# Kernel tuning notes

Hardware: AMD Instinct MI355X
Metric: run time of the kernel (lower is better)

Reference implementation:

```python
import jax, jax.numpy as jnp
import numpy as np
from jax import lax

T, B, A_DIM, Z_DIM, K_MIX, HID = 128, 256, 16, 32, 8, 128
Q_REG = 1e-3
R_REG = 1e-3


def setup_inputs() -> dict:
    key = jax.random.key(0)
    ks = jax.random.split(key, 16)
    s = 1.0 / np.sqrt(HID)
    reg = 0.9
    as_ = jax.random.normal(ks[0], (T, B, A_DIM), dtype=jnp.float32)
    mat_A_K = (1.0 - reg) * jax.random.normal(ks[1], (K_MIX, Z_DIM, Z_DIM)) + reg * jnp.eye(Z_DIM)
    mat_C_K = (1.0 - reg) * jax.random.normal(ks[2], (K_MIX, A_DIM, Z_DIM)) + reg * jnp.eye(A_DIM, Z_DIM)
    # Cholesky factors of near-identity SPD matrices (as in torch init)
    Q_L = jnp.tril(0.05 * jax.random.normal(ks[3], (Z_DIM, Z_DIM))) + jnp.eye(Z_DIM)
    R_L = jnp.tril(0.05 * jax.random.normal(ks[4], (A_DIM, A_DIM))) + jnp.eye(A_DIM)
    init_mean = jnp.zeros((Z_DIM,), dtype=jnp.float32)
    init_cov = jnp.eye(Z_DIM, dtype=jnp.float32)
    u = lambda k, shp: jax.random.uniform(k, shp, minval=-s, maxval=s, dtype=jnp.float32)
    return dict(
        as_=as_, mat_A_K=mat_A_K, mat_C_K=mat_C_K, Q_L=Q_L, R_L=R_L,
        init_mean=init_mean, init_cov=init_cov,
        W_ih0=u(ks[5], (4 * HID, A_DIM)), W_hh0=u(ks[6], (4 * HID, HID)),
        b_ih0=u(ks[7], (4 * HID,)), b_hh0=u(ks[8], (4 * HID,)),
        W_ih1=u(ks[9], (4 * HID, HID)), W_hh1=u(ks[10], (4 * HID, HID)),
        b_ih1=u(ks[11], (4 * HID,)), b_hh1=u(ks[12], (4 * HID,)),
        W_out=u(ks[13], (K_MIX, HID)), b_out=u(ks[14], (K_MIX,)),
    )


def _lstm_cell(x, h, c, W_ih, W_hh, b_ih, b_hh):
    g = x @ W_ih.T + b_ih + h @ W_hh.T + b_hh
    i, f, gg, o = jnp.split(g, 4, axis=-1)
    c2 = jax.nn.sigmoid(f) * c + jax.nn.sigmoid(i) * jnp.tanh(gg)
    h2 = jax.nn.sigmoid(o) * jnp.tanh(c2)
    return h2, c2


def reference(as_, mat_A_K, mat_C_K, Q_L, R_L, init_mean, init_cov,
              W_ih0, W_hh0, b_ih0, b_hh0, W_ih1, W_hh1, b_ih1, b_hh1,
              W_out, b_out):
    Tn, Bn, a_dim = as_.shape
    Kn, z_dim, _ = mat_A_K.shape
    Hn = W_hh0.shape[1]
    Q = Q_L @ Q_L.T + Q_REG * jnp.eye(z_dim, dtype=as_.dtype)
    R = R_L @ R_L.T + R_REG * jnp.eye(a_dim, dtype=as_.dtype)

    def weight_model(a, h0, c0, h1, c1):
        h0, c0 = _lstm_cell(a, h0, c0, W_ih0, W_hh0, b_ih0, b_hh0)
        h1, c1 = _lstm_cell(h0, h1, c1, W_ih1, W_hh1, b_ih1, b_hh1)
        w = jax.nn.softmax(h1 @ W_out.T + b_out, axis=-1)
        return w, h0, c0, h1, c1

    def step(carry, a_t):
        mean_p, cov_p, weight, h0, c0, h1, c1 = carry
        # mixture matrices for this step (weight == previous step's w_next; ones at t=0)
        mat_A = jnp.einsum('bk,kij->bij', weight, mat_A_K)
        mat_C = jnp.einsum('bk,kij->bij', weight, mat_C_K)
        # sample_control = ('mean','mean'), observation_mask=None -> a = as_[t]
        w_next, h0, c0, h1, c1 = weight_model(a_t, h0, c0, h1, c1)
        mat_A_next = jnp.einsum('bk,kij->bij', w_next, mat_A_K)
        CP = mat_C @ cov_p                                   # (B,a,z)
        S = CP @ jnp.swapaxes(mat_C, 1, 2) + R               # (B,a,a)
        K_t = cov_p @ jnp.swapaxes(mat_C, 1, 2) @ jnp.linalg.inv(S)
        mean_t = mean_p + K_t @ (a_t[..., None] - mat_C @ mean_p)
        mean_p2 = mat_A_next @ mean_t
        cov_t = cov_p - K_t @ CP
        cov_t = 0.5 * (cov_t + jnp.swapaxes(cov_t, 1, 2))
        cov_p2 = mat_A_next @ cov_t @ jnp.swapaxes(mat_A_next, 1, 2) + Q
        cov_p2 = 0.5 * (cov_p2 + jnp.swapaxes(cov_p2, 1, 2))
        new_carry = (mean_p2, cov_p2, w_next, h0, c0, h1, c1)
        outs = (mean_t, cov_t, mean_p2, cov_p2, mat_A, mat_C, a_t)
        return new_carry, outs

    init = (
        jnp.broadcast_to(init_mean[None, :, None], (Bn, z_dim, 1)),
        jnp.broadcast_to(init_cov[None], (Bn, z_dim, z_dim)),
        jnp.ones((Bn, Kn), dtype=as_.dtype),
        jnp.zeros((Bn, Hn), dtype=as_.dtype), jnp.zeros((Bn, Hn), dtype=as_.dtype),
        jnp.zeros((Bn, Hn), dtype=as_.dtype), jnp.zeros((Bn, Hn), dtype=as_.dtype),
    )
    carry, ys = lax.scan(step, init, as_)
    means, covs, next_means, next_covs, mat_As, mat_Cs, a_seq = ys
    w_fin = carry[2]
    mat_A_fin = jnp.einsum('bk,kij->bij', w_fin, mat_A_K)
    mat_C_fin = jnp.einsum('bk,kij->bij', w_fin, mat_C_K)
    mat_As = jnp.concatenate([mat_As, mat_A_fin[None]], axis=0)   # (T+1,B,z,z)
    mat_Cs = jnp.concatenate([mat_Cs, mat_C_fin[None]], axis=0)   # (T+1,B,a,z)
    a_out = a_seq[:, None]                                        # (T,1,B,a) as in torch stack
    return means, covs, next_means, next_covs, mat_As, mat_Cs, a_out
```

## Files before the change

kernel.cpp:

```cpp
#include <hip/hip_runtime.h>
#include <hip/hip_fp16.h>
#include <math.h>

#define T_STEPS 128
#define B_SZ 256
#define AD 16
#define ZD 32
#define KM 8
#define HID 128
#define G4H 512
#define NTHR 512

#define WS_WQ   0
#define WS_WI0  98304
#define WS_BS0  102400
#define WS_BS1  102912
#define WS_Q    103424
#define WS_R    104448

typedef float f32x4 __attribute__((ext_vector_type(4)));

__device__ __forceinline__ unsigned pk16(float lo, float hi) {
  unsigned a = __half_as_ushort(__float2half_rn(lo));
  unsigned b = __half_as_ushort(__float2half_rn(hi));
  return a | (b << 16);
}

__global__ void ssm_prep_kernel(const float* __restrict__ Wih0, const float* __restrict__ Whh0,
                                const float* __restrict__ Wih1, const float* __restrict__ Whh1,
                                const float* __restrict__ bih0, const float* __restrict__ bhh0,
                                const float* __restrict__ bih1, const float* __restrict__ bhh1,
                                const float* __restrict__ QL, const float* __restrict__ RL,
                                float* __restrict__ ws) {
  unsigned* wsu = (unsigned*)ws;
  int tid = blockIdx.x * blockDim.x + threadIdx.x;
  int nt = gridDim.x * blockDim.x;
  for (int j = tid; j < G4H; j += nt) {
    for (int d4 = 0; d4 < 48; ++d4) {
      for (int m = 0; m < 4; ++m) {
        int dd = (d4 & 15) * 4 + m;
        const float* src = (d4 < 16) ? Whh0 : (d4 < 32) ? Wih1 : Whh1;
        wsu[WS_WQ + (d4 * 512 + j) * 4 + m] =
            pk16(src[j * 128 + 2 * dd], src[j * 128 + 2 * dd + 1]);
      }
    }
    for (int k = 0; k < 8; ++k)
      wsu[WS_WI0 + k * 512 + j] = pk16(Wih0[j * 16 + 2 * k], Wih0[j * 16 + 2 * k + 1]);
    ws[WS_BS0 + j] = bih0[j] + bhh0[j];
    ws[WS_BS1 + j] = bih1[j] + bhh1[j];
  }
  for (int e = tid; e < ZD * ZD; e += nt) {
    int i = e >> 5, j = e & 31;
    float s = 0.f;
    for (int k = 0; k < ZD; ++k) s += QL[i * ZD + k] * QL[j * ZD + k];
    if (i == j) s += 0.001f;
    ws[WS_Q + e] = s;
  }
  for (int e = tid; e < AD * AD; e += nt) {
    int i = e >> 4, j = e & 15;
    float s = 0.f;
    for (int k = 0; k < AD; ++k) s += RL[i * AD + k] * RL[j * AD + k];
    if (i == j) s += 0.001f;
    ws[WS_R + e] = s;
  }
}

__device__ __forceinline__ float sigm(float x) { return 1.0f / (1.0f + expf(-x)); }
__device__ __forceinline__ float dotv(f32x4 a, f32x4 b) {
  return a[0] * b[0] + a[1] * b[1] + a[2] * b[2] + a[3] * b[3];
}
__device__ __forceinline__ void st_nt(float* p, float v) { __builtin_nontemporal_store(v, p); }
__device__ __forceinline__ void st_nt4(float* p, f32x4 v) {
  __builtin_nontemporal_store(v, (f32x4*)p);
}

__device__ __forceinline__ float dot2f(unsigned a, unsigned b, float c) {
#if __has_builtin(__builtin_amdgcn_fdot2)
  typedef _Float16 h2 __attribute__((ext_vector_type(2)));
  union U { unsigned u; h2 h; };
  U ua, ub; ua.u = a; ub.u = b;
  return __builtin_amdgcn_fdot2(ua.h, ub.h, c, false);
#else
  union U { unsigned u; _Float16 h[2]; };
  U ua, ub; ua.u = a; ub.u = b;
  return c + (float)ua.h[0] * (float)ub.h[0] + (float)ua.h[1] * (float)ub.h[1];
#endif
}

struct alignas(16) LS {
  unsigned ap[8];
  unsigned h0p[64];
  unsigned h1p[64];
  float g[G4H];
  float lgp[16];
};

__global__ void __launch_bounds__(NTHR, 2) ssm_lstm_kernel(
    const float* __restrict__ as_, const float* __restrict__ AK, const float* __restrict__ CK,
    const float* __restrict__ Wout, const float* __restrict__ bout,
    const float* __restrict__ ws, float* __restrict__ out) {
  __shared__ LS s;
  const int tid = threadIdx.x;
  const int b = blockIdx.x;
  const unsigned* wsu = (const unsigned*)ws;
  const uint4* Wg = (const uint4*)(wsu + WS_WQ);
  const f32x4* AK4 = (const f32x4*)AK;
  const f32x4* CK4 = (const f32x4*)CK;

  float* o_As = out + (size_t)T_STEPS * B_SZ * ZD + (size_t)T_STEPS * B_SZ * ZD * ZD +
                (size_t)T_STEPS * B_SZ * ZD + (size_t)T_STEPS * B_SZ * ZD * ZD;
  float* o_Cs = o_As + (size_t)(T_STEPS + 1) * B_SZ * ZD * ZD;
  float* o_a = o_Cs + (size_t)(T_STEPS + 1) * B_SZ * AD * ZD;

  const uint4* h0p4 = (const uint4*)s.h0p;
  const uint4* h1p4 = (const uint4*)s.h1p;
  const uint4* ap4 = (const uint4*)s.ap;

  unsigned wi0r[8];
  #pragma unroll
  for (int k = 0; k < 8; ++k) wi0r[k] = wsu[WS_WI0 + k * 512 + tid];
  const float bs0r = ws[WS_BS0 + tid];
  const float bs1r = ws[WS_BS1 + tid];
  float woutr[8];
  #pragma unroll
  for (int gi = 0; gi < KM; ++gi) woutr[gi] = (tid < HID) ? Wout[gi * HID + tid] : 0.f;
  float boutr[8];
  #pragma unroll
  for (int k = 0; k < KM; ++k) boutr[k] = bout[k];

  float c0r = 0.f, c1r = 0.f;

  if (tid < 64) { s.h0p[tid] = 0u; s.h1p[tid] = 0u; }
  if (tid < AD) {
    float v = as_[(size_t)b * AD + tid];
    ((__half*)s.ap)[tid] = __float2half_rn(v);
    st_nt(&o_a[(size_t)b * AD + tid], v);
  }
  if (tid < 256) {
    f32x4 acc = {0.f, 0.f, 0.f, 0.f};
    #pragma unroll
    for (int k = 0; k < KM; ++k) acc += AK4[k * 256 + tid];
    st_nt4(&o_As[(size_t)b * 1024 + tid * 4], acc);
  } else if (tid < 384) {
    int idx = tid - 256;
    f32x4 acc = {0.f, 0.f, 0.f, 0.f};
    #pragma unroll
    for (int k = 0; k < KM; ++k) acc += CK4[k * 128 + idx];
    st_nt4(&o_Cs[(size_t)b * 512 + idx * 4], acc);
  }
  __syncthreads();

  for (int t = 0; t < T_STEPS; ++t) {
    const size_t tb2 = (size_t)(t + 1) * B_SZ + b;

    {
      float acc = bs0r;
      #pragma unroll
      for (int k4 = 0; k4 < 2; ++k4) {
        uint4 av = ap4[k4];
        acc = dot2f(av.x, wi0r[k4 * 4 + 0], acc);
        acc = dot2f(av.y, wi0r[k4 * 4 + 1], acc);
        acc = dot2f(av.z, wi0r[k4 * 4 + 2], acc);
        acc = dot2f(av.w, wi0r[k4 * 4 + 3], acc);
      }
      #pragma unroll
      for (int d4 = 0; d4 < 16; ++d4) {
        uint4 w = Wg[d4 * 512 + tid];
        uint4 hv = h0p4[d4];
        acc = dot2f(hv.x, w.x, acc);
        acc = dot2f(hv.y, w.y, acc);
        acc = dot2f(hv.z, w.z, acc);
        acc = dot2f(hv.w, w.w, acc);
      }
      s.g[tid] = acc;
    }
    __syncthreads();

    if (tid < HID) {
      float ig = sigm(s.g[tid]);
      float fg = sigm(s.g[HID + tid]);
      float gg = tanhf(s.g[2 * HID + tid]);
      float og = sigm(s.g[3 * HID + tid]);
      c0r = fg * c0r + ig * gg;
      ((__half*)s.h0p)[tid] = __float2half_rn(og * tanhf(c0r));
    }
    __syncthreads();

    {
      float acc = bs1r;
      #pragma unroll
      for (int d4 = 0; d4 < 16; ++d4) {
        uint4 w = Wg[(16 + d4) * 512 + tid];
        uint4 hv = h0p4[d4];
        acc = dot2f(hv.x, w.x, acc);
        acc = dot2f(hv.y, w.y, acc);
        acc = dot2f(hv.z, w.z, acc);
        acc = dot2f(hv.w, w.w, acc);
      }
      #pragma unroll
      for (int d4 = 0; d4 < 16; ++d4) {
        uint4 w = Wg[(32 + d4) * 512 + tid];
        uint4 hv = h1p4[d4];
        acc = dot2f(hv.x, w.x, acc);
        acc = dot2f(hv.y, w.y, acc);
        acc = dot2f(hv.z, w.z, acc);
        acc = dot2f(hv.w, w.w, acc);
      }
      s.g[tid] = acc;
    }
    __syncthreads();

    if (tid < HID) {
      float ig = sigm(s.g[tid]);
      float fg = sigm(s.g[HID + tid]);
      float gg = tanhf(s.g[2 * HID + tid]);
      float og = sigm(s.g[3 * HID + tid]);
      c1r = fg * c1r + ig * gg;
      float h1u = og * tanhf(c1r);
      ((__half*)s.h1p)[tid] = __float2half_rn(h1u);
      int w2 = tid >> 6, lane = tid & 63;
      #pragma unroll
      for (int gi = 0; gi < KM; ++gi) {
        float p = woutr[gi] * h1u;
        #pragma unroll
        for (int m = 32; m >= 1; m >>= 1) p += __shfl_xor(p, m);
        if (lane == 0) s.lgp[w2 * KM + gi] = p;
      }
    }
    __syncthreads();

    {
      float lg[KM];
      float mx = -1e30f;
      #pragma unroll
      for (int k = 0; k < KM; ++k) {
        lg[k] = s.lgp[k] + s.lgp[KM + k] + boutr[k];
        mx = fmaxf(mx, lg[k]);
      }
      float sum = 0.f;
      #pragma unroll
      for (int k = 0; k < KM; ++k) { lg[k] = expf(lg[k] - mx); sum += lg[k]; }
      float inv = 1.0f / sum;
      #pragma unroll
      for (int k = 0; k < KM; ++k) lg[k] *= inv;
      if (tid < 256) {
        f32x4 acc = {0.f, 0.f, 0.f, 0.f};
        #pragma unroll
        for (int k = 0; k < KM; ++k) acc += lg[k] * AK4[k * 256 + tid];
        st_nt4(&o_As[tb2 * 1024 + tid * 4], acc);
      } else if (tid < 384) {
        int idx = tid - 256;
        f32x4 acc = {0.f, 0.f, 0.f, 0.f};
        #pragma unroll
        for (int k = 0; k < KM; ++k) acc += lg[k] * CK4[k * 128 + idx];
        st_nt4(&o_Cs[tb2 * 512 + idx * 4], acc);
      } else if (tid >= 448 && tid < 448 + AD && t < T_STEPS - 1) {
        int i = tid - 448;
        float v = as_[tb2 * AD + i];
        ((__half*)s.ap)[i] = __float2half_rn(v);
        st_nt(&o_a[tb2 * AD + i], v);
      }
    }
    __syncthreads();
  }
}

struct alignas(16) KS {
  float P[ZD * 36];
  float An[ZD * 36];
  float Mt[ZD * 36];
  float MtT[ZD * 36];
  float Sy[ZD * 36];
  float ACt[ZD * 36];
  float Qs[ZD * 36];
  float C[AD * 36];
  float Aug[AD * 52];
  float Kk[ZD * 20];
  float Rs[AD * AD];
  float meanp[ZD], meant[ZD], r[AD], af[AD];
};

__global__ void __launch_bounds__(256, 1) ssm_kalman_kernel(
    const float* __restrict__ as_, const float* __restrict__ initm,
    const float* __restrict__ initc, const float* __restrict__ ws,
    float* __restrict__ out) {
  __shared__ KS s;
  const int l = threadIdx.x;
  const int b = blockIdx.x;
  const int i32 = l & 31, cq = l >> 5;
  const int i16 = l & 15, j16 = l >> 4;

  float* o_means = out;
  float* o_covs = o_means + (size_t)T_STEPS * B_SZ * ZD;
  float* o_nmean = o_covs + (size_t)T_STEPS * B_SZ * ZD * ZD;
  float* o_ncovs = o_nmean + (size_t)T_STEPS * B_SZ * ZD;
  const float* o_As = o_ncovs + (size_t)T_STEPS * B_SZ * ZD * ZD;
  const float* o_Cs = o_As + (size_t)(T_STEPS + 1) * B_SZ * ZD * ZD;

  f32x4* P4 = (f32x4*)s.P;
  f32x4* An4 = (f32x4*)s.An;
  f32x4* Mt4 = (f32x4*)s.Mt;
  f32x4* MtT4 = (f32x4*)s.MtT;
  f32x4* Sy4 = (f32x4*)s.Sy;
  f32x4* ACt4 = (f32x4*)s.ACt;
  f32x4* Q4 = (f32x4*)s.Qs;
  f32x4* C4 = (f32x4*)s.C;
  f32x4* Aug4 = (f32x4*)s.Aug;
  f32x4* Kk4 = (f32x4*)s.Kk;
  f32x4* af4 = (f32x4*)s.af;
  const f32x4* r4 = (const f32x4*)s.r;
  const f32x4* meanp4 = (const f32x4*)s.meanp;
  const f32x4* meant4 = (const f32x4*)s.meant;

  #pragma unroll
  for (int q = 0; q < 4; ++q) {
    int e = q * 256 + l;
    s.P[(e >> 5) * 36 + (e & 31)] = initc[e];
    s.Qs[(e >> 5) * 36 + (e & 31)] = ws[WS_Q + e];
  }
  s.Rs[l] = ws[WS_R + l];
  if (l < ZD) s.meanp[l] = initm[l];
  {
    const f32x4* gc = (const f32x4*)&o_Cs[(size_t)b * 512];
    if (l < 128) C4[(l >> 3) * 9 + (l & 7)] = gc[l];
    const f32x4* ga = (const f32x4*)&o_As[((size_t)B_SZ + b) * 1024];
    An4[(l >> 3) * 9 + (l & 7)] = ga[l];
    if (l < 4) af4[l] = ((const f32x4*)&as_[(size_t)b * AD])[l];
  }
  __syncthreads();

  for (int t = 0; t < T_STEPS; ++t) {
    const size_t tb = (size_t)t * B_SZ + b;
    const bool pf = (t < T_STEPS - 1);

    f32x4 pfC = {0, 0, 0, 0};
    f32x4 pfA = {0, 0, 0, 0};
    f32x4 pfa = {0, 0, 0, 0};
    if (pf) {
      if (l >= 128) pfC = ((const f32x4*)&o_Cs[(tb + B_SZ) * 512])[l - 128];
      pfA = ((const f32x4*)&o_As[(tb + 2 * B_SZ) * 1024])[l];
      if (l < 4) pfa = ((const f32x4*)&as_[(tb + B_SZ) * AD])[l];
    }

    {
      float a0 = 0.f, a1 = 0.f;
      #pragma unroll
      for (int k4 = 0; k4 < 8; ++k4) {
        f32x4 cr = C4[i16 * 9 + k4];
        a0 += dotv(cr, P4[j16 * 9 + k4]);
        a1 += dotv(cr, P4[(j16 + 16) * 9 + k4]);
      }
      s.Aug[i16 * 52 + AD + j16] = a0;
      s.Aug[i16 * 52 + AD + j16 + 16] = a1;
    }
    __syncthreads();

    {
      float acc = s.Rs[i16 * AD + j16];
      #pragma unroll
      for (int k4 = 0; k4 < 8; ++k4)
        acc += dotv(Aug4[i16 * 13 + 4 + k4], C4[j16 * 9 + k4]);
      s.Aug[i16 * 52 + j16] = acc;
      if (l >= 240) {
        int ii = l - 240;
        float rr = s.af[ii];
        #pragma unroll
        for (int k4 = 0; k4 < 8; ++k4) rr -= dotv(C4[ii * 9 + k4], meanp4[k4]);
        s.r[ii] = rr;
      }
    }
    __syncthreads();

    if (l < 64) {
      const int lc = (l < 48) ? l : 47;
      float col[16];
      #pragma unroll
      for (int i = 0; i < AD; ++i) col[i] = s.Aug[i * 52 + lc];
      #pragma unroll
      for (int j = 0; j < AD; ++j) {
        float pd = __shfl(col[j], j);
        float pinv = 1.0f / pd;
        float oldj = col[j];
        #pragma unroll
        for (int i = 0; i < AD; ++i) {
          if (i == j) continue;
          float fi = __shfl(col[i], j);
          col[i] = fmaf(-(fi * pinv), oldj, col[i]);
        }
        col[j] = oldj * pinv;
      }
      if (l >= AD && l < AD + ZD) {
        int rr = l - AD;
        f32x4 v0 = {col[0], col[1], col[2], col[3]};
        f32x4 v1 = {col[4], col[5], col[6], col[7]};
        f32x4 v2 = {col[8], col[9], col[10], col[11]};
        f32x4 v3 = {col[12], col[13], col[14], col[15]};
        Kk4[rr * 5 + 0] = v0;
        Kk4[rr * 5 + 1] = v1;
        Kk4[rr * 5 + 2] = v2;
        Kk4[rr * 5 + 3] = v3;
      }
    } else if (pf && l >= 128) {
      int idx = l - 128;
      C4[(idx >> 3) * 9 + (idx & 7)] = pfC;
    }
    __syncthreads();

    {
      f32x4 acc = {0.f, 0.f, 0.f, 0.f};
      #pragma unroll
      for (int k4 = 0; k4 < 4; ++k4) {
        f32x4 kv = Kk4[i32 * 5 + k4];
        #pragma unroll
        for (int kk = 0; kk < 4; ++kk) {
          f32x4 cpk = Aug4[(4 * k4 + kk) * 13 + 4 + cq];
          acc += kv[kk] * cpk;
        }
      }
      f32x4 mv = P4[i32 * 9 + cq] - acc;
      Mt4[i32 * 9 + cq] = mv;
      #pragma unroll
      for (int jj = 0; jj < 4; ++jj) s.MtT[(4 * cq + jj) * 36 + i32] = mv[jj];
    }
    __syncthreads();

    {
      f32x4 sv = 0.5f * (Mt4[i32 * 9 + cq] + MtT4[i32 * 9 + cq]);
      Sy4[i32 * 9 + cq] = sv;
      st_nt4(&o_covs[tb * 1024 + i32 * 32 + cq * 4], sv);
      if (l < ZD) {
        float acc = s.meanp[l];
        #pragma unroll
        for (int m = 0; m < 4; ++m) acc += dotv(Kk4[l * 5 + m], r4[m]);
        s.meant[l] = acc;
        st_nt(&o_means[tb * ZD + l], acc);
      }
    }
    __syncthreads();

    {
      float c0 = 0.f, c1 = 0.f, c2 = 0.f, c3 = 0.f;
      #pragma unroll
      for (int k4 = 0; k4 < 8; ++k4) {
        f32x4 an = An4[i32 * 9 + k4];
        c0 += dotv(an, Sy4[(4 * cq + 0) * 9 + k4]);
        c1 += dotv(an, Sy4[(4 * cq + 1) * 9 + k4]);
        c2 += dotv(an, Sy4[(4 * cq + 2) * 9 + k4]);
        c3 += dotv(an, Sy4[(4 * cq + 3) * 9 + k4]);
      }
      f32x4 v = {c0, c1, c2, c3};
      ACt4[i32 * 9 + cq] = v;
    }
    __syncthreads();

    {
      if (l < ZD) {
        float acc = 0.f;
        #pragma unroll
        for (int k4 = 0; k4 < 8; ++k4) acc += dotv(An4[l * 9 + k4], meant4[k4]);
        s.meanp[l] = acc;
        st_nt(&o_nmean[tb * ZD + l], acc);
      }
      float c0 = 0.f, c1 = 0.f, c2 = 0.f, c3 = 0.f;
      #pragma unroll
      for (int k4 = 0; k4 < 8; ++k4) {
        f32x4 ac = ACt4[i32 * 9 + k4];
        c0 += dotv(ac, An4[(4 * cq + 0) * 9 + k4]);
        c1 += dotv(ac, An4[(4 * cq + 1) * 9 + k4]);
        c2 += dotv(ac, An4[(4 * cq + 2) * 9 + k4]);
        c3 += dotv(ac, An4[(4 * cq + 3) * 9 + k4]);
      }
      f32x4 mv = {c0, c1, c2, c3};
      Mt4[i32 * 9 + cq] = mv;
      #pragma unroll
      for (int jj = 0; jj < 4; ++jj) s.MtT[(4 * cq + jj) * 36 + i32] = mv[jj];
    }
    __syncthreads();

    {
      f32x4 pv = 0.5f * (Mt4[i32 * 9 + cq] + MtT4[i32 * 9 + cq]) + Q4[i32 * 9 + cq];
      P4[i32 * 9 + cq] = pv;
      st_nt4(&o_ncovs[tb * 1024 + i32 * 32 + cq * 4], pv);
    }
    __syncthreads();

    if (pf) {
      An4[(l >> 3) * 9 + (l & 7)] = pfA;
      if (l < 4) af4[l] = pfa;
    }
    __syncthreads();
  }
}

extern "C" void kernel_launch(void* const* d_in, const int* in_sizes, int n_in,
                              void* d_out, int out_size, void* d_ws, size_t ws_size,
                              hipStream_t stream) {
  const float* as_ = (const float*)d_in[0];
  const float* AK = (const float*)d_in[1];
  const float* CK = (const float*)d_in[2];
  const float* QL = (const float*)d_in[3];
  const float* RL = (const float*)d_in[4];
  const float* initm = (const float*)d_in[5];
  const float* initc = (const float*)d_in[6];
  const float* Wih0 = (const float*)d_in[7];
  const float* Whh0 = (const float*)d_in[8];
  const float* bih0 = (const float*)d_in[9];
  const float* bhh0 = (const float*)d_in[10];
  const float* Wih1 = (const float*)d_in[11];
  const float* Whh1 = (const float*)d_in[12];
  const float* bih1 = (const float*)d_in[13];
  const float* bhh1 = (const float*)d_in[14];
  const float* Wout = (const float*)d_in[15];
  const float* bout = (const float*)d_in[16];
  float* ws = (float*)d_ws;
  float* out = (float*)d_out;

  ssm_prep_kernel<<<16, 256, 0, stream>>>(Wih0, Whh0, Wih1, Whh1, bih0, bhh0, bih1, bhh1,
                                          QL, RL, ws);
  ssm_lstm_kernel<<<B_SZ, NTHR, 0, stream>>>(as_, AK, CK, Wout, bout, ws, out);
  ssm_kalman_kernel<<<B_SZ, 256, 0, stream>>>(as_, initm, initc, ws, out);
}
```

Before: 1.588 ms.

## Fuse LSTM and Kalman kernels with per-batch progress flags for overlap

```diff
diff --git a/kernel.cpp b/kernel.cpp
--- a/kernel.cpp
+++ b/kernel.cpp
@@ -17,6 +17,7 @@
 #define WS_BS1  102912
 #define WS_Q    103424
 #define WS_R    104448
+#define WS_PROG 104704
 
 typedef float f32x4 __attribute__((ext_vector_type(4)));
 
@@ -35,6 +36,7 @@
   unsigned* wsu = (unsigned*)ws;
   int tid = blockIdx.x * blockDim.x + threadIdx.x;
   int nt = gridDim.x * blockDim.x;
+  for (int e = tid; e < B_SZ; e += nt) ((int*)ws)[WS_PROG + e] = 0;
   for (int j = tid; j < G4H; j += nt) {
     for (int d4 = 0; d4 < 48; ++d4) {
       for (int m = 0; m < 4; ++m) {
@@ -95,176 +97,6 @@
   float lgp[16];
 };
 
-__global__ void __launch_bounds__(NTHR, 2) ssm_lstm_kernel(
-    const float* __restrict__ as_, const float* __restrict__ AK, const float* __restrict__ CK,
-    const float* __restrict__ Wout, const float* __restrict__ bout,
-    const float* __restrict__ ws, float* __restrict__ out) {
-  __shared__ LS s;
-  const int tid = threadIdx.x;
-  const int b = blockIdx.x;
-  const unsigned* wsu = (const unsigned*)ws;
-  const uint4* Wg = (const uint4*)(wsu + WS_WQ);
-  const f32x4* AK4 = (const f32x4*)AK;
-  const f32x4* CK4 = (const f32x4*)CK;
-
-  float* o_As = out + (size_t)T_STEPS * B_SZ * ZD + (size_t)T_STEPS * B_SZ * ZD * ZD +
-                (size_t)T_STEPS * B_SZ * ZD + (size_t)T_STEPS * B_SZ * ZD * ZD;
-  float* o_Cs = o_As + (size_t)(T_STEPS + 1) * B_SZ * ZD * ZD;
-  float* o_a = o_Cs + (size_t)(T_STEPS + 1) * B_SZ * AD * ZD;
-
-  const uint4* h0p4 = (const uint4*)s.h0p;
-  const uint4* h1p4 = (const uint4*)s.h1p;
-  const uint4* ap4 = (const uint4*)s.ap;
-
-  unsigned wi0r[8];
-  #pragma unroll
-  for (int k = 0; k < 8; ++k) wi0r[k] = wsu[WS_WI0 + k * 512 + tid];
-  const float bs0r = ws[WS_BS0 + tid];
-  const float bs1r = ws[WS_BS1 + tid];
-  float woutr[8];
-  #pragma unroll
-  for (int gi = 0; gi < KM; ++gi) woutr[gi] = (tid < HID) ? Wout[gi * HID + tid] : 0.f;
-  float boutr[8];
-  #pragma unroll
-  for (int k = 0; k < KM; ++k) boutr[k] = bout[k];
-
-  float c0r = 0.f, c1r = 0.f;
-
-  if (tid < 64) { s.h0p[tid] = 0u; s.h1p[tid] = 0u; }
-  if (tid < AD) {
-    float v = as_[(size_t)b * AD + tid];
-    ((__half*)s.ap)[tid] = __float2half_rn(v);
-    st_nt(&o_a[(size_t)b * AD + tid], v);
-  }
-  if (tid < 256) {
-    f32x4 acc = {0.f, 0.f, 0.f, 0.f};
-    #pragma unroll
-    for (int k = 0; k < KM; ++k) acc += AK4[k * 256 + tid];
-    st_nt4(&o_As[(size_t)b * 1024 + tid * 4], acc);
-  } else if (tid < 384) {
-    int idx = tid - 256;
-    f32x4 acc = {0.f, 0.f, 0.f, 0.f};
-    #pragma unroll
-    for (int k = 0; k < KM; ++k) acc += CK4[k * 128 + idx];
-    st_nt4(&o_Cs[(size_t)b * 512 + idx * 4], acc);
-  }
-  __syncthreads();
-
-  for (int t = 0; t < T_STEPS; ++t) {
-    const size_t tb2 = (size_t)(t + 1) * B_SZ + b;
-
-    {
-      float acc = bs0r;
-      #pragma unroll
-      for (int k4 = 0; k4 < 2; ++k4) {
-        uint4 av = ap4[k4];
-        acc = dot2f(av.x, wi0r[k4 * 4 + 0], acc);
-        acc = dot2f(av.y, wi0r[k4 * 4 + 1], acc);
-        acc = dot2f(av.z, wi0r[k4 * 4 + 2], acc);
-        acc = dot2f(av.w, wi0r[k4 * 4 + 3], acc);
-      }
-      #pragma unroll
-      for (int d4 = 0; d4 < 16; ++d4) {
-        uint4 w = Wg[d4 * 512 + tid];
-        uint4 hv = h0p4[d4];
-        acc = dot2f(hv.x, w.x, acc);
-        acc = dot2f(hv.y, w.y, acc);
-        acc = dot2f(hv.z, w.z, acc);
-        acc = dot2f(hv.w, w.w, acc);
-      }
-      s.g[tid] = acc;
-    }
-    __syncthreads();
-
-    if (tid < HID) {
-      float ig = sigm(s.g[tid]);
-      float fg = sigm(s.g[HID + tid]);
-      float gg = tanhf(s.g[2 * HID + tid]);
-      float og = sigm(s.g[3 * HID + tid]);
-      c0r = fg * c0r + ig * gg;
-      ((__half*)s.h0p)[tid] = __float2half_rn(og * tanhf(c0r));
-    }
-    __syncthreads();
-
-    {
-      float acc = bs1r;
-      #pragma unroll
-      for (int d4 = 0; d4 < 16; ++d4) {
-        uint4 w = Wg[(16 + d4) * 512 + tid];
-        uint4 hv = h0p4[d4];
-        acc = dot2f(hv.x, w.x, acc);
-        acc = dot2f(hv.y, w.y, acc);
-        acc = dot2f(hv.z, w.z, acc);
-        acc = dot2f(hv.w, w.w, acc);
-      }
-      #pragma unroll
-      for (int d4 = 0; d4 < 16; ++d4) {
-        uint4 w = Wg[(32 + d4) * 512 + tid];
-        uint4 hv = h1p4[d4];
-        acc = dot2f(hv.x, w.x, acc);
-        acc = dot2f(hv.y, w.y, acc);
-        acc = dot2f(hv.z, w.z, acc);
-        acc = dot2f(hv.w, w.w, acc);
-      }
-      s.g[tid] = acc;
-    }
-    __syncthreads();
-
-    if (tid < HID) {
-      float ig = sigm(s.g[tid]);
-      float fg = sigm(s.g[HID + tid]);
-      float gg = tanhf(s.g[2 * HID + tid]);
-      float og = sigm(s.g[3 * HID + tid]);
-      c1r = fg * c1r + ig * gg;
-      float h1u = og * tanhf(c1r);
-      ((__half*)s.h1p)[tid] = __float2half_rn(h1u);
-      int w2 = tid >> 6, lane = tid & 63;
-      #pragma unroll
-      for (int gi = 0; gi < KM; ++gi) {
-        float p = woutr[gi] * h1u;
-        #pragma unroll
-        for (int m = 32; m >= 1; m >>= 1) p += __shfl_xor(p, m);
-        if (lane == 0) s.lgp[w2 * KM + gi] = p;
-      }
-    }
-    __syncthreads();
-
-    {
-      float lg[KM];
-      float mx = -1e30f;
-      #pragma unroll
-      for (int k = 0; k < KM; ++k) {
-        lg[k] = s.lgp[k] + s.lgp[KM + k] + boutr[k];
-        mx = fmaxf(mx, lg[k]);
-      }
-      float sum = 0.f;
-      #pragma unroll
-      for (int k = 0; k < KM; ++k) { lg[k] = expf(lg[k] - mx); sum += lg[k]; }
-      float inv = 1.0f / sum;
-      #pragma unroll
-      for (int k = 0; k < KM; ++k) lg[k] *= inv;
-      if (tid < 256) {
-        f32x4 acc = {0.f, 0.f, 0.f, 0.f};
-        #pragma unroll
-        for (int k = 0; k < KM; ++k) acc += lg[k] * AK4[k * 256 + tid];
-        st_nt4(&o_As[tb2 * 1024 + tid * 4], acc);
-      } else if (tid < 384) {
-        int idx = tid - 256;
-        f32x4 acc = {0.f, 0.f, 0.f, 0.f};
-        #pragma unroll
-        for (int k = 0; k < KM; ++k) acc += lg[k] * CK4[k * 128 + idx];
-        st_nt4(&o_Cs[tb2 * 512 + idx * 4], acc);
-      } else if (tid >= 448 && tid < 448 + AD && t < T_STEPS - 1) {
-        int i = tid - 448;
-        float v = as_[tb2 * AD + i];
-        ((__half*)s.ap)[i] = __float2half_rn(v);
-        st_nt(&o_a[tb2 * AD + i], v);
-      }
-    }
-    __syncthreads();
-  }
-}
-
 struct alignas(16) KS {
   float P[ZD * 36];
   float An[ZD * 36];
@@ -280,22 +112,193 @@
   float meanp[ZD], meant[ZD], r[AD], af[AD];
 };
 
-__global__ void __launch_bounds__(256, 1) ssm_kalman_kernel(
-    const float* __restrict__ as_, const float* __restrict__ initm,
-    const float* __restrict__ initc, const float* __restrict__ ws,
-    float* __restrict__ out) {
-  __shared__ KS s;
-  const int l = threadIdx.x;
-  const int b = blockIdx.x;
-  const int i32 = l & 31, cq = l >> 5;
-  const int i16 = l & 15, j16 = l >> 4;
+union SMEM { LS ls; KS ks; };
+
+__global__ void __launch_bounds__(NTHR, 2) ssm_fused_kernel(
+    const float* __restrict__ as_, const float* __restrict__ AK, const float* __restrict__ CK,
+    const float* __restrict__ Wout, const float* __restrict__ bout,
+    const float* __restrict__ initm, const float* __restrict__ initc,
+    float* __restrict__ ws, float* __restrict__ out) {
+  __shared__ SMEM sm;
+  const int tid = threadIdx.x;
+  const unsigned* wsu = (const unsigned*)ws;
+  int* prog = (int*)ws + WS_PROG;
 
   float* o_means = out;
   float* o_covs = o_means + (size_t)T_STEPS * B_SZ * ZD;
   float* o_nmean = o_covs + (size_t)T_STEPS * B_SZ * ZD * ZD;
   float* o_ncovs = o_nmean + (size_t)T_STEPS * B_SZ * ZD;
-  const float* o_As = o_ncovs + (size_t)T_STEPS * B_SZ * ZD * ZD;
-  const float* o_Cs = o_As + (size_t)(T_STEPS + 1) * B_SZ * ZD * ZD;
+  float* o_As = o_ncovs + (size_t)T_STEPS * B_SZ * ZD * ZD;
+  float* o_Cs = o_As + (size_t)(T_STEPS + 1) * B_SZ * ZD * ZD;
+  float* o_a = o_Cs + (size_t)(T_STEPS + 1) * B_SZ * AD * ZD;
+
+  if (blockIdx.x < B_SZ) {
+    LS& s = sm.ls;
+    const int b = blockIdx.x;
+    const uint4* Wg = (const uint4*)(wsu + WS_WQ);
+    const f32x4* AK4 = (const f32x4*)AK;
+    const f32x4* CK4 = (const f32x4*)CK;
+    const uint4* h0p4 = (const uint4*)s.h0p;
+    const uint4* h1p4 = (const uint4*)s.h1p;
+    const uint4* ap4 = (const uint4*)s.ap;
+
+    unsigned wi0r[8];
+    #pragma unroll
+    for (int k = 0; k < 8; ++k) wi0r[k] = wsu[WS_WI0 + k * 512 + tid];
+    const float bs0r = ws[WS_BS0 + tid];
+    const float bs1r = ws[WS_BS1 + tid];
+    float woutr[8];
+    #pragma unroll
+    for (int gi = 0; gi < KM; ++gi) woutr[gi] = (tid < HID) ? Wout[gi * HID + tid] : 0.f;
+    float boutr[8];
+    #pragma unroll
+    for (int k = 0; k < KM; ++k) boutr[k] = bout[k];
+
+    float c0r = 0.f, c1r = 0.f;
+
+    if (tid < 64) { s.h0p[tid] = 0u; s.h1p[tid] = 0u; }
+    if (tid < AD) {
+      float v = as_[(size_t)b * AD + tid];
+      ((__half*)s.ap)[tid] = __float2half_rn(v);
+      st_nt(&o_a[(size_t)b * AD + tid], v);
+    }
+    if (tid < 256) {
+      f32x4 acc = {0.f, 0.f, 0.f, 0.f};
+      #pragma unroll
+      for (int k = 0; k < KM; ++k) acc += AK4[k * 256 + tid];
+      st_nt4(&o_As[(size_t)b * 1024 + tid * 4], acc);
+    } else if (tid < 384) {
+      int idx = tid - 256;
+      f32x4 acc = {0.f, 0.f, 0.f, 0.f};
+      #pragma unroll
+      for (int k = 0; k < KM; ++k) acc += CK4[k * 128 + idx];
+      st_nt4(&o_Cs[(size_t)b * 512 + idx * 4], acc);
+    }
+    __syncthreads();
+
+    for (int t = 0; t < T_STEPS; ++t) {
+      const size_t tb2 = (size_t)(t + 1) * B_SZ + b;
+
+      {
+        float acc = bs0r;
+        #pragma unroll
+        for (int k4 = 0; k4 < 2; ++k4) {
+          uint4 av = ap4[k4];
+          acc = dot2f(av.x, wi0r[k4 * 4 + 0], acc);
+          acc = dot2f(av.y, wi0r[k4 * 4 + 1], acc);
+          acc = dot2f(av.z, wi0r[k4 * 4 + 2], acc);
+          acc = dot2f(av.w, wi0r[k4 * 4 + 3], acc);
+        }
+        #pragma unroll
+        for (int d4 = 0; d4 < 16; ++d4) {
+          uint4 w = Wg[d4 * 512 + tid];
+          uint4 hv = h0p4[d4];
+          acc = dot2f(hv.x, w.x, acc);
+          acc = dot2f(hv.y, w.y, acc);
+          acc = dot2f(hv.z, w.z, acc);
+          acc = dot2f(hv.w, w.w, acc);
+        }
+        s.g[tid] = acc;
+      }
+      __syncthreads();
+
+      if (tid < HID) {
+        float ig = sigm(s.g[tid]);
+        float fg = sigm(s.g[HID + tid]);
+        float gg = tanhf(s.g[2 * HID + tid]);
+        float og = sigm(s.g[3 * HID + tid]);
+        c0r = fg * c0r + ig * gg;
+        ((__half*)s.h0p)[tid] = __float2half_rn(og * tanhf(c0r));
+      }
+      __syncthreads();
+
+      {
+        float acc = bs1r;
+        #pragma unroll
+        for (int d4 = 0; d4 < 16; ++d4) {
+          uint4 w = Wg[(16 + d4) * 512 + tid];
+          uint4 hv = h0p4[d4];
+          acc = dot2f(hv.x, w.x, acc);
+          acc = dot2f(hv.y, w.y, acc);
+          acc = dot2f(hv.z, w.z, acc);
+          acc = dot2f(hv.w, w.w, acc);
+        }
+        #pragma unroll
+        for (int d4 = 0; d4 < 16; ++d4) {
+          uint4 w = Wg[(32 + d4) * 512 + tid];
+          uint4 hv = h1p4[d4];
+          acc = dot2f(hv.x, w.x, acc);
+          acc = dot2f(hv.y, w.y, acc);
+          acc = dot2f(hv.z, w.z, acc);
+          acc = dot2f(hv.w, w.w, acc);
+        }
+        s.g[tid] = acc;
+      }
+      __syncthreads();
+
+      if (tid < HID) {
+        float ig = sigm(s.g[tid]);
+        float fg = sigm(s.g[HID + tid]);
+        float gg = tanhf(s.g[2 * HID + tid]);
+        float og = sigm(s.g[3 * HID + tid]);
+        c1r = fg * c1r + ig * gg;
+        float h1u = og * tanhf(c1r);
+        ((__half*)s.h1p)[tid] = __float2half_rn(h1u);
+        int w2 = tid >> 6, lane = tid & 63;
+        #pragma unroll
+        for (int gi = 0; gi < KM; ++gi) {
+          float p = woutr[gi] * h1u;
+          #pragma unroll
+          for (int m = 32; m >= 1; m >>= 1) p += __shfl_xor(p, m);
+          if (lane == 0) s.lgp[w2 * KM + gi] = p;
+        }
+      }
+      __syncthreads();
+
+      {
+        float lg[KM];
+        float mx = -1e30f;
+        #pragma unroll
+        for (int k = 0; k < KM; ++k) {
+          lg[k] = s.lgp[k] + s.lgp[KM + k] + boutr[k];
+          mx = fmaxf(mx, lg[k]);
+        }
+        float sum = 0.f;
+        #pragma unroll
+        for (int k = 0; k < KM; ++k) { lg[k] = expf(lg[k] - mx); sum += lg[k]; }
+        float inv = 1.0f / sum;
+        #pragma unroll
+        for (int k = 0; k < KM; ++k) lg[k] *= inv;
+        if (tid < 256) {
+          f32x4 acc = {0.f, 0.f, 0.f, 0.f};
+          #pragma unroll
+          for (int k = 0; k < KM; ++k) acc += lg[k] * AK4[k * 256 + tid];
+          st_nt4(&o_As[tb2 * 1024 + tid * 4], acc);
+        } else if (tid < 384) {
+          int idx = tid - 256;
+          f32x4 acc = {0.f, 0.f, 0.f, 0.f};
+          #pragma unroll
+          for (int k = 0; k < KM; ++k) acc += lg[k] * CK4[k * 128 + idx];
+          st_nt4(&o_Cs[tb2 * 512 + idx * 4], acc);
+        } else if (tid >= 448 && tid < 448 + AD && t < T_STEPS - 1) {
+          int i = tid - 448;
+          float v = as_[tb2 * AD + i];
+          ((__half*)s.ap)[i] = __float2half_rn(v);
+          st_nt(&o_a[tb2 * AD + i], v);
+        }
+      }
+      __syncthreads();
+      if (tid == 0)
+        __hip_atomic_store(&prog[b], t + 1, __ATOMIC_RELEASE, __HIP_MEMORY_SCOPE_AGENT);
+    }
+    return;
+  }
+
+  KS& s = sm.ks;
+  const int b = blockIdx.x - B_SZ;
+  const int l = tid;
+  const int i32 = l & 31, cq = (l & 255) >> 5;
+  const int i16 = l & 15, j16 = (l & 255) >> 4;
 
   f32x4* P4 = (f32x4*)s.P;
   f32x4* An4 = (f32x4*)s.An;
@@ -312,20 +315,15 @@
   const f32x4* meanp4 = (const f32x4*)s.meanp;
   const f32x4* meant4 = (const f32x4*)s.meant;
 
-  #pragma unroll
-  for (int q = 0; q < 4; ++q) {
-    int e = q * 256 + l;
-    s.P[(e >> 5) * 36 + (e & 31)] = initc[e];
-    s.Qs[(e >> 5) * 36 + (e & 31)] = ws[WS_Q + e];
-  }
-  s.Rs[l] = ws[WS_R + l];
-  if (l < ZD) s.meanp[l] = initm[l];
-  {
-    const f32x4* gc = (const f32x4*)&o_Cs[(size_t)b * 512];
-    if (l < 128) C4[(l >> 3) * 9 + (l & 7)] = gc[l];
-    const f32x4* ga = (const f32x4*)&o_As[((size_t)B_SZ + b) * 1024];
-    An4[(l >> 3) * 9 + (l & 7)] = ga[l];
-    if (l < 4) af4[l] = ((const f32x4*)&as_[(size_t)b * AD])[l];
+  if (l < 256) {
+    #pragma unroll
+    for (int q = 0; q < 4; ++q) {
+      int e = q * 256 + l;
+      s.P[(e >> 5) * 36 + (e & 31)] = initc[e];
+      s.Qs[(e >> 5) * 36 + (e & 31)] = ws[WS_Q + e];
+    }
+    s.Rs[l] = ws[WS_R + l];
+    if (l < ZD) s.meanp[l] = initm[l];
   }
   __syncthreads();
 
@@ -333,16 +331,35 @@
     const size_t tb = (size_t)t * B_SZ + b;
     const bool pf = (t < T_STEPS - 1);
 
+    if (tid == 0) {
+      int need = pf ? (t + 2) : T_STEPS;
+      if (need > T_STEPS) need = T_STEPS;
+      int spins = 0;
+      while (__hip_atomic_load(&prog[b], __ATOMIC_ACQUIRE, __HIP_MEMORY_SCOPE_AGENT) < need) {
+        __builtin_amdgcn_s_sleep(16);
+        if (++spins > 1000000) break;
+      }
+    }
+    __syncthreads();
+
+    if (t == 0) {
+      if (l < 128) C4[(l >> 3) * 9 + (l & 7)] = ((const f32x4*)&o_Cs[(size_t)b * 512])[l];
+      if (l < 256) An4[(l >> 3) * 9 + (l & 7)] =
+          ((const f32x4*)&o_As[((size_t)B_SZ + b) * 1024])[l];
+      if (l < 4) af4[l] = ((const f32x4*)&as_[(size_t)b * AD])[l];
+      __syncthreads();
+    }
+
     f32x4 pfC = {0, 0, 0, 0};
     f32x4 pfA = {0, 0, 0, 0};
     f32x4 pfa = {0, 0, 0, 0};
-    if (pf) {
+    if (pf && l < 256) {
       if (l >= 128) pfC = ((const f32x4*)&o_Cs[(tb + B_SZ) * 512])[l - 128];
       pfA = ((const f32x4*)&o_As[(tb + 2 * B_SZ) * 1024])[l];
       if (l < 4) pfa = ((const f32x4*)&as_[(tb + B_SZ) * AD])[l];
     }
 
-    {
+    if (l < 256) {
       float a0 = 0.f, a1 = 0.f;
       #pragma unroll
       for (int k4 = 0; k4 < 8; ++k4) {
@@ -355,7 +372,7 @@
     }
     __syncthreads();
 
-    {
+    if (l < 256) {
       float acc = s.Rs[i16 * AD + j16];
       #pragma unroll
       for (int k4 = 0; k4 < 8; ++k4)
@@ -400,13 +417,13 @@
         Kk4[rr * 5 + 2] = v2;
         Kk4[rr * 5 + 3] = v3;
       }
-    } else if (pf && l >= 128) {
+    } else if (pf && l >= 128 && l < 256) {
       int idx = l - 128;
       C4[(idx >> 3) * 9 + (idx & 7)] = pfC;
     }
     __syncthreads();
 
-    {
+    if (l < 256) {
       f32x4 acc = {0.f, 0.f, 0.f, 0.f};
       #pragma unroll
       for (int k4 = 0; k4 < 4; ++k4) {
@@ -424,7 +441,7 @@
     }
     __syncthreads();
 
-    {
+    if (l < 256) {
       f32x4 sv = 0.5f * (Mt4[i32 * 9 + cq] + MtT4[i32 * 9 + cq]);
       Sy4[i32 * 9 + cq] = sv;
       st_nt4(&o_covs[tb * 1024 + i32 * 32 + cq * 4], sv);
@@ -438,7 +455,7 @@
     }
     __syncthreads();
 
-    {
+    if (l < 256) {
       float c0 = 0.f, c1 = 0.f, c2 = 0.f, c3 = 0.f;
       #pragma unroll
       for (int k4 = 0; k4 < 8; ++k4) {
@@ -453,7 +470,7 @@
     }
     __syncthreads();
 
-    {
+    if (l < 256) {
       if (l < ZD) {
         float acc = 0.f;
         #pragma unroll
@@ -477,14 +494,14 @@
     }
     __syncthreads();
 
-    {
+    if (l < 256) {
       f32x4 pv = 0.5f * (Mt4[i32 * 9 + cq] + MtT4[i32 * 9 + cq]) + Q4[i32 * 9 + cq];
       P4[i32 * 9 + cq] = pv;
       st_nt4(&o_ncovs[tb * 1024 + i32 * 32 + cq * 4], pv);
     }
     __syncthreads();
 
-    if (pf) {
+    if (pf && l < 256) {
       An4[(l >> 3) * 9 + (l & 7)] = pfA;
       if (l < 4) af4[l] = pfa;
     }
@@ -517,6 +534,6 @@
 
   ssm_prep_kernel<<<16, 256, 0, stream>>>(Wih0, Whh0, Wih1, Whh1, bih0, bhh0, bih1, bhh1,
                                           QL, RL, ws);
-  ssm_lstm_kernel<<<B_SZ, NTHR, 0, stream>>>(as_, AK, CK, Wout, bout, ws, out);
-  ssm_kalman_kernel<<<B_SZ, 256, 0, stream>>>(as_, initm, initc, ws, out);
-}
+  ssm_fused_kernel<<<2 * B_SZ, NTHR, 0, stream>>>(as_, AK, CK, Wout, bout, initm, initc,
+                                                  ws, out);
+}
```

After: 2.644 ms. 66.5% more time.
